# Kernel optimization log

Hardware: AMD Instinct MI355X
Metric: run time of the kernel (lower is better)

Reference implementation:

```python
import jax, jax.numpy as jnp
import numpy as np

NUM_CLASSES = 80
IOU_THR = 0.5
SCORE_THR = 0.3
K = 256              # per-class candidate pool (pre-NMS top-k)
MAX_PER_CLASS = 100  # max_output_size_per_class
MAX_TOTAL = 100      # max_total_size
NEG = -1e9


def _make_boxes(key, shape):
    kc, ks = jax.random.split(key)
    cyx = jax.random.uniform(kc, shape + (2,), dtype=jnp.float32)
    hw = jax.random.uniform(ks, shape + (2,), dtype=jnp.float32) * 0.2
    return jnp.concatenate([cyx - hw * 0.5, cyx + hw * 0.5], axis=-1)  # [y1,x1,y2,x2]


def setup_inputs() -> dict:
    key = jax.random.key(0)
    ks = jax.random.split(key, 9)
    B = 8
    inp = {}
    for i, g in enumerate([52, 26, 13]):
        inp[f"b{i+1}"] = _make_boxes(ks[3 * i], (B, g, g, 3))                       # (B,g,g,3,4)
        inp[f"c{i+1}"] = jax.random.uniform(ks[3 * i + 1], (B, g, g, 3, 1))          # objectness
        inp[f"p{i+1}"] = jax.random.uniform(ks[3 * i + 2], (B, g, g, 3, NUM_CLASSES))
    return inp


def _pairwise_iou(b):  # b: (K,4) in [y1,x1,y2,x2]
    y1, x1, y2, x2 = b[:, 0], b[:, 1], b[:, 2], b[:, 3]
    area = (y2 - y1) * (x2 - x1)
    iy = jnp.clip(jnp.minimum(y2[:, None], y2[None, :]) - jnp.maximum(y1[:, None], y1[None, :]), 0.0)
    ix = jnp.clip(jnp.minimum(x2[:, None], x2[None, :]) - jnp.maximum(x1[:, None], x1[None, :]), 0.0)
    inter = iy * ix
    union = area[:, None] + area[None, :] - inter
    return jnp.where(union > 0, inter / union, 0.0)


def _nms_one_class(boxes, scores):  # boxes (N,4), scores (N,)
    sc, idx = jax.lax.top_k(scores, K)
    b = boxes[idx]                      # (K,4) sorted by score desc
    valid = sc > SCORE_THR
    iou = _pairwise_iou(b)              # (K,K)
    rng = jnp.arange(K)

    def body(keep, i):
        cur = keep[i] & valid[i]
        keep = keep & ~(cur & (iou[i] > IOU_THR) & (rng > i))
        return keep, cur

    _, kept = jax.lax.scan(body, jnp.ones(K, dtype=bool), rng)
    kept = kept & (jnp.cumsum(kept) <= MAX_PER_CLASS)
    return b, jnp.where(kept, sc, NEG)  # (K,4), (K,)


def _combined_nms(boxes, scores):  # boxes (B,N,4), scores (B,N,C)
    per_class = jax.vmap(_nms_one_class, in_axes=(None, 1))   # over classes
    per_image = jax.vmap(per_class, in_axes=(0, 0))           # over batch
    cb, cs = per_image(boxes, scores)                         # (B,C,K,4), (B,C,K)
    B, C = scores.shape[0], scores.shape[2]
    flat_s = cs.reshape(B, C * K)
    flat_b = cb.reshape(B, C * K, 4)
    cls_ids = jnp.broadcast_to(jnp.arange(C, dtype=jnp.float32)[:, None], (C, K)).reshape(C * K)
    top_s, top_i = jax.lax.top_k(flat_s, MAX_TOTAL)           # global top-100
    top_b = jnp.take_along_axis(flat_b, top_i[:, :, None], axis=1)
    top_c = cls_ids[top_i]
    valid = top_s > SCORE_THR
    boxes_out = jnp.clip(jnp.where(valid[..., None], top_b, 0.0), 0.0, 1.0)  # clip_boxes=True
    scores_out = jnp.where(valid, top_s, 0.0)
    classes_out = jnp.where(valid, top_c, 0.0)
    nvalid = valid.sum(axis=-1).astype(jnp.int32)
    return boxes_out, scores_out, classes_out, nvalid


def reference(b1, c1, p1, b2, c2, p2, b3, c3, p3):
    B = b1.shape[0]
    bboxes = jnp.concatenate([b.reshape(B, -1, 4) for b in (b1, b2, b3)], axis=1)          # (B,N,4)
    conf = jnp.concatenate([c.reshape(B, -1, 1) for c in (c1, c2, c3)], axis=1)            # (B,N,1)
    cls = jnp.concatenate([p.reshape(B, -1, NUM_CLASSES) for p in (p1, p2, p3)], axis=1)   # (B,N,C)
    scores = conf * cls                                                                     # (B,N,C)
    return _combined_nms(bboxes, scores)
```

## Files before the change

### kernel.cpp

```cpp
#include <hip/hip_runtime.h>
#include <stdint.h>

#define BATCH 8
#define NC 80
#define NA1 8112
#define NA2 2028
#define NA3 507
#define NTOT 10647
#define TILE 64
#define NTILES 167
#define NSLOTS (NTILES*TILE)
#define KSEL 256
#define MAXPC 100
#define MAXTOT 100
#define SCTHR 0.3f
#define IOUTHR 0.5f
#define KEYTHR 0xBE99999Au
#define KEYBASE 0xBE99999Bu
#define STAGE_CAP 5120

typedef unsigned long long ull;

__device__ ull g_cand[(size_t)BATCH * NC * NSLOTS];
__device__ unsigned g_tcnt[BATCH * NC * NTILES];
__device__ ull g_ks[BATCH * NC * MAXPC];
__device__ unsigned g_kcnt[BATCH * NC];
__device__ ull g_ms[BATCH * 10 * MAXTOT];
__device__ unsigned g_mcnt[BATCH * 10];

__device__ __forceinline__ unsigned okey(float f) {
  unsigned u = __float_as_uint(f);
  return u ^ ((unsigned)((int)u >> 31) | 0x80000000u);
}
__device__ __forceinline__ float inv_okey(unsigned k) {
  unsigned u = (k & 0x80000000u) ? (k ^ 0x80000000u) : ~k;
  return __uint_as_float(u);
}
__device__ __forceinline__ ull shflxor64(ull v, int m) {
  int lo = __shfl_xor((int)(unsigned)v, m, 64);
  int hi = __shfl_xor((int)(unsigned)(v >> 32), m, 64);
  return ((ull)(unsigned)hi << 32) | (unsigned)lo;
}
__device__ __forceinline__ ull bcast64(ull v, int src) {
  int lo = __shfl((int)(unsigned)v, src, 64);
  int hi = __shfl((int)(unsigned)(v >> 32), src, 64);
  return ((ull)(unsigned)hi << 32) | (unsigned)lo;
}
__device__ __forceinline__ unsigned wave_sufscan(unsigned v, int lane) {
  #pragma unroll
  for (int off = 1; off < 64; off <<= 1) {
    unsigned t = __shfl_down(v, off, 64);
    if (lane + off < 64) v += t;
  }
  return v;
}

template <typename F>
__device__ void radix_sel24(F getkey, int n, unsigned kwant,
                            unsigned* hist4, unsigned* suf,
                            unsigned* s_sel, unsigned* wtot,
                            unsigned& T_out, unsigned& need_out)
{
  const int tid = threadIdx.x;
  const int lane = tid & 63, wv = tid >> 6;
  const int wb = wv << 8;
  unsigned need = kwant, prefix = 0;
  for (int shift = 16; shift >= 0; shift -= 8) {
    hist4[tid] = 0; hist4[tid + 256] = 0; hist4[tid + 512] = 0; hist4[tid + 768] = 0;
    __syncthreads();
    unsigned maskhi = (shift == 16) ? 0u : (0x00FFFFFFu ^ ((1u << (shift + 8)) - 1u));
    for (int i = tid; i < n; i += 256) {
      unsigned k = getkey(i);
      if (k != 0xFFFFFFFFu && (k & maskhi) == prefix)
        atomicAdd(&hist4[wb + ((k >> shift) & 255u)], 1u);
    }
    __syncthreads();
    unsigned v = hist4[tid] + hist4[tid + 256] + hist4[tid + 512] + hist4[tid + 768];
    v = wave_sufscan(v, lane);
    if (lane == 0) wtot[wv] = v;
    __syncthreads();
    unsigned add = 0;
    for (int w = wv + 1; w < 4; ++w) add += wtot[w];
    v += add;
    suf[tid] = v;
    __syncthreads();
    unsigned nxt = (tid == 255) ? 0u : suf[tid + 1];
    if (v >= need && nxt < need) {
      s_sel[0] = prefix | ((unsigned)tid << shift);
      s_sel[1] = need - nxt;
    }
    __syncthreads();
    prefix = s_sel[0]; need = s_sel[1];
    __syncthreads();
  }
  T_out = prefix; need_out = need;
}

__global__ __launch_bounds__(256)
void score_compact(const float* __restrict__ c1, const float* __restrict__ p1,
                   const float* __restrict__ c2, const float* __restrict__ p2,
                   const float* __restrict__ c3, const float* __restrict__ p3)
{
  const int tid = threadIdx.x;
  const int b = blockIdx.x / NTILES;
  const int t = blockIdx.x % NTILES;
  const int n0 = t * TILE;

  __shared__ float sp[TILE * 81];

  for (int e4 = tid; e4 < TILE * 20; e4 += 256) {
    int a = e4 / 20;
    int c4 = (e4 - a * 20) * 4;
    int ng = n0 + a;
    if (ng < NTOT) {
      const float* pp; int nl;
      if (ng < NA1)            { pp = p1 + (size_t)b * NA1 * NC; nl = ng; }
      else if (ng < NA1 + NA2) { pp = p2 + (size_t)b * NA2 * NC; nl = ng - NA1; }
      else                     { pp = p3 + (size_t)b * NA3 * NC; nl = ng - NA1 - NA2; }
      float4 pv = *(const float4*)(pp + (size_t)nl * NC + c4);
      sp[a * 81 + c4 + 0] = pv.x; sp[a * 81 + c4 + 1] = pv.y;
      sp[a * 81 + c4 + 2] = pv.z; sp[a * 81 + c4 + 3] = pv.w;
    }
  }
  __syncthreads();

  const int wv = tid >> 6, lane = tid & 63;
  const int ng = n0 + lane;
  const bool av = ng < NTOT;
  float cf = 0.0f;
  if (av) {
    if (ng < NA1)            cf = c1[b * NA1 + ng];
    else if (ng < NA1 + NA2) cf = c2[b * NA2 + ng - NA1];
    else                     cf = c3[b * NA3 + ng - NA1 - NA2];
  }
  for (int k = 0; k < 20; ++k) {
    int c = wv + 4 * k;
    float pv = av ? sp[lane * 81 + c] : 0.0f;
    unsigned key = okey(pv * cf);
    bool pred = av && (key > KEYTHR);
    ull m = __ballot(pred);
    if (pred) {
      unsigned pos = (unsigned)__popcll(m & ((1ull << lane) - 1ull));
      g_cand[((size_t)(b * NC + c) * NTILES + t) * TILE + pos] =
          ((ull)key << 32) | (unsigned)(~ng);
    }
    if (lane == 0) g_tcnt[(b * NC + c) * NTILES + t] = (unsigned)__popcll(m);
  }
}

__global__ __launch_bounds__(256)
void nms_per_class(const float* __restrict__ b1, const float* __restrict__ b2,
                   const float* __restrict__ b3)
{
  const int tid = threadIdx.x;
  const int lane = tid & 63, wv = tid >> 6;
  const int bc = blockIdx.x;
  const int b = bc / NC;
  const int c = bc - b * NC;

  __shared__ unsigned ckey[STAGE_CAP];
  __shared__ unsigned short cslot[STAGE_CAP];
  __shared__ ull uSupp[KSEL * 5];
  __shared__ float4 cbox[KSEL];
  __shared__ ull cand[KSEL];
  __shared__ ull kw[4], kfw[4];
  __shared__ unsigned s_sel[2], wtot[4];
  __shared__ int s_cgt, s_ceq;

  ull* supp = uSupp;
  unsigned* hist4 = (unsigned*)uSupp;
  unsigned* suf = (unsigned*)uSupp + 1024;
  unsigned* tc = (unsigned*)cbox;
  unsigned* off = (unsigned*)cbox + 168;

  const ull* crow = g_cand + (size_t)bc * NSLOTS;
  const unsigned* trow = g_tcnt + bc * NTILES;

  cand[tid] = 0ull;
  if (tid < NTILES) tc[tid] = trow[tid];
  __syncthreads();

  if (wv == 0) {
    unsigned carry = 0;
    for (int ch = 0; ch < 3; ++ch) {
      int idx = ch * 64 + lane;
      unsigned x = (idx < NTILES) ? tc[idx] : 0u;
      unsigned v = x;
      #pragma unroll
      for (int o = 1; o < 64; o <<= 1) {
        unsigned t2 = __shfl_up(v, o, 64);
        if (lane >= o) v += t2;
      }
      if (idx < NTILES) off[idx] = carry + v - x;
      carry += (unsigned)__shfl((int)v, 63, 64);
    }
    if (lane == 0) off[NTILES] = carry;
  }
  __syncthreads();
  const int cnt = (int)off[NTILES];
  const bool staged = (cnt > KSEL) && (cnt <= STAGE_CAP);

  for (int s = tid; s < NSLOTS; s += 256) {
    int t = s >> 6, j = s & 63;
    if (j < (int)tc[t]) {
      if (cnt <= KSEL) {
        cand[off[t] + j] = crow[s];
      } else if (staged) {
        int pos = off[t] + j;
        ckey[pos] = (unsigned)(crow[s] >> 32);
        cslot[pos] = (unsigned short)s;
      }
    }
  }
  __syncthreads();

  if (cnt > KSEL) {
    unsigned T, need;
    if (staged) {
      auto gk = [&](int i) { return ckey[i] - KEYBASE; };
      radix_sel24(gk, cnt, KSEL, hist4, suf, s_sel, wtot, T, need);
    } else {
      auto gk = [&](int s) {
        int t = s >> 6, j = s & 63;
        return (j < (int)tc[t]) ? ((unsigned)(crow[s] >> 32) - KEYBASE) : 0xFFFFFFFFu;
      };
      radix_sel24(gk, NSLOTS, KSEL, hist4, suf, s_sel, wtot, T, need);
    }
    if (tid == 0) { s_cgt = 0; s_ceq = 0; }
    __syncthreads();
    const int ngt = KSEL - (int)need;
    if (staged) {
      for (int i = tid; i < cnt; i += 256) {
        unsigned k = ckey[i] - KEYBASE;
        if (k > T) cand[atomicAdd(&s_cgt, 1)] = crow[cslot[i]];
        else if (k == T) { int p = atomicAdd(&s_ceq, 1); if (p < (int)need) cand[ngt + p] = crow[cslot[i]]; }
      }
    } else {
      for (int s = tid; s < NSLOTS; s += 256) {
        int t = s >> 6, j = s & 63;
        if (j < (int)tc[t]) {
          ull v = crow[s];
          unsigned k = (unsigned)(v >> 32) - KEYBASE;
          if (k > T) cand[atomicAdd(&s_cgt, 1)] = v;
          else if (k == T) { int p = atomicAdd(&s_ceq, 1); if (p < (int)need) cand[ngt + p] = v; }
        }
      }
    }
  }
  __syncthreads();

  ull v = cand[tid];
  for (int kk = 2; kk <= KSEL; kk <<= 1) {
    for (int j = kk >> 1; j > 0; j >>= 1) {
      ull o;
      if (j >= 64) {
        cand[tid] = v;
        __syncthreads();
        o = cand[tid ^ j];
        __syncthreads();
      } else {
        o = shflxor64(v, j);
      }
      bool keep_max = (((tid & j) == 0) == ((tid & kk) == 0));
      v = keep_max ? (v > o ? v : o) : (v < o ? v : o);
    }
  }
  __syncthreads();

  int myn = 0;
  {
    float4 bx = make_float4(0.f, 0.f, 0.f, 0.f);
    if (v != 0ull) {
      myn = (int)(~(unsigned)v);
      const float* bp;
      if (myn < NA1)            bp = b1 + (size_t)(b * NA1 + myn) * 4;
      else if (myn < NA1 + NA2) bp = b2 + (size_t)(b * NA2 + (myn - NA1)) * 4;
      else                      bp = b3 + (size_t)(b * NA3 + (myn - NA1 - NA2)) * 4;
      bx = make_float4(bp[0], bp[1], bp[2], bp[3]);
    }
    cbox[tid] = bx;
  }
  ull mvalid = __ballot(v != 0ull);
  if (lane == 0) kw[wv] = mvalid;
  __syncthreads();

  {
    const float4 mb = cbox[tid];
    const float myarea = (mb.z - mb.x) * (mb.w - mb.y);
    ull m0 = 0, m1 = 0, m2 = 0, m3 = 0;
    for (int j = 0; j < KSEL; ++j) {
      float4 bj = cbox[j];
      float ja = (bj.z - bj.x) * (bj.w - bj.y);
      float iy = fmaxf(fminf(bj.z, mb.z) - fmaxf(bj.x, mb.x), 0.0f);
      float ix = fmaxf(fminf(bj.w, mb.w) - fmaxf(bj.y, mb.y), 0.0f);
      float inter = iy * ix;
      float uni = ja + myarea - inter;
      bool sup = (j > tid) && (uni > 0.0f) && (inter > IOUTHR * uni);
      ull bit = sup ? (1ull << (j & 63)) : 0ull;
      if ((j >> 6) == 0) m0 |= bit; else if ((j >> 6) == 1) m1 |= bit;
      else if ((j >> 6) == 2) m2 |= bit; else m3 |= bit;
    }
    supp[tid * 5 + 0] = m0; supp[tid * 5 + 1] = m1;
    supp[tid * 5 + 2] = m2; supp[tid * 5 + 3] = m3;
  }
  __syncthreads();

  if (wv == 0) {
    ull r0[4], r1[4], r2[4], r3[4];
    #pragma unroll
    for (int w = 0; w < 4; ++w) {
      r0[w] = supp[(lane) * 5 + w];
      r1[w] = supp[(64 + lane) * 5 + w];
      r2[w] = supp[(128 + lane) * 5 + w];
      r3[w] = supp[(192 + lane) * 5 + w];
    }
    ull k0 = kw[0], k1 = kw[1], k2 = kw[2], k3 = kw[3];
    ull f0 = 0, f1 = 0, f2 = 0, f3 = 0;
    int run = 0;
#define SCAN_CHUNK(R, KT, FT)                                              \
    for (int ib = 0; ib < 64; ++ib) {                                      \
      if ((KT >> ib) & 1ull) {                                             \
        k0 &= ~bcast64(R[0], ib); k1 &= ~bcast64(R[1], ib);                \
        k2 &= ~bcast64(R[2], ib); k3 &= ~bcast64(R[3], ib);                \
        if (++run <= MAXPC) FT |= (1ull << ib);                            \
      }                                                                    \
    }
    SCAN_CHUNK(r0, k0, f0)
    SCAN_CHUNK(r1, k1, f1)
    SCAN_CHUNK(r2, k2, f2)
    SCAN_CHUNK(r3, k3, f3)
#undef SCAN_CHUNK
    if (lane == 0) { kfw[0] = f0; kfw[1] = f1; kfw[2] = f2; kfw[3] = f3; }
  }
  __syncthreads();

  {
    ull w0 = kfw[0], w1 = kfw[1], w2 = kfw[2], w3 = kfw[3];
    int wq = tid >> 6, wb2 = tid & 63;
    ull myw = (wq == 0) ? w0 : (wq == 1) ? w1 : (wq == 2) ? w2 : w3;
    bool kept = (myw >> wb2) & 1ull;
    if (kept) {
      ull lt = (wb2 == 0) ? 0ull : (myw & ((1ull << wb2) - 1ull));
      int rank = __popcll(lt);
      if (wq > 0) rank += __popcll(w0);
      if (wq > 1) rank += __popcll(w1);
      if (wq > 2) rank += __popcll(w2);
      unsigned key = (unsigned)(v >> 32);
      unsigned n = (~(unsigned)v) & 0x3FFFu;
      ull e = ((ull)(key - KEYBASE) << 40) | ((ull)(unsigned)(127 - c) << 33) |
              ((ull)(unsigned)(255 - tid) << 25) | n;
      g_ks[(size_t)bc * MAXPC + rank] = e;
    }
    if (tid == 0)
      g_kcnt[bc] = (unsigned)(__popcll(w0) + __popcll(w1) + __popcll(w2) + __popcll(w3));
  }
}

__global__ __launch_bounds__(256)
void nms_merge8()
{
  const int tid = threadIdx.x;
  const int b = blockIdx.x / 10, g = blockIdx.x % 10;
  __shared__ ull le[8 * MAXPC];
  __shared__ ull cand[128];
  __shared__ unsigned kc[8], ko[9];
  __shared__ unsigned hist4[1024], suf[256], s_sel[2], wtot[4];
  __shared__ int s_cgt, s_ceq;

  if (tid < 8) kc[tid] = g_kcnt[b * NC + g * 8 + tid];
  if (tid < 128) cand[tid] = 0ull;
  __syncthreads();
  if (tid == 0) { unsigned a = 0; for (int i = 0; i < 8; ++i) { ko[i] = a; a += kc[i]; } ko[8] = a; }
  __syncthreads();
  const int total = (int)ko[8];

  for (int s = tid; s < 8 * MAXPC; s += 256) {
    int c8 = s / MAXPC, j = s - c8 * MAXPC;
    if (j < (int)kc[c8]) le[ko[c8] + j] = g_ks[(size_t)(b * NC + g * 8 + c8) * MAXPC + j];
  }
  __syncthreads();

  if (total <= MAXTOT) {
    if (tid < total) cand[tid] = le[tid];
  } else {
    unsigned T, need;
    auto gk = [&](int i) { return (unsigned)(le[i] >> 40); };
    radix_sel24(gk, total, MAXTOT, hist4, suf, s_sel, wtot, T, need);
    if (tid == 0) { s_cgt = 0; s_ceq = 0; }
    __syncthreads();
    const int ngt = MAXTOT - (int)need;
    for (int i = tid; i < total; i += 256) {
      unsigned k = (unsigned)(le[i] >> 40);
      if (k > T) cand[atomicAdd(&s_cgt, 1)] = le[i];
      else if (k == T) { int p = atomicAdd(&s_ceq, 1); if (p < (int)need) cand[ngt + p] = le[i]; }
    }
  }
  __syncthreads();

  for (int kk = 2; kk <= 128; kk <<= 1) {
    for (int j = kk >> 1; j > 0; j >>= 1) {
      if (tid < 128) {
        int ixj = tid ^ j;
        if (ixj > tid) {
          ull a = cand[tid], c2 = cand[ixj];
          if (((tid & kk) == 0) ? (a < c2) : (a > c2)) { cand[tid] = c2; cand[ixj] = a; }
        }
      }
      __syncthreads();
    }
  }
  if (tid < MAXTOT) g_ms[(size_t)(b * 10 + g) * MAXTOT + tid] = cand[tid];
  if (tid == 0) g_mcnt[b * 10 + g] = (unsigned)(total < MAXTOT ? total : MAXTOT);
}

__global__ __launch_bounds__(256)
void nms_final(const float* __restrict__ b1, const float* __restrict__ b2,
               const float* __restrict__ b3, float* __restrict__ out)
{
  const int tid = threadIdx.x;
  const int b = blockIdx.x;
  __shared__ ull me[10 * MAXTOT];
  __shared__ ull cand[128];
  __shared__ unsigned mc[10], mo[11];
  __shared__ unsigned hist4[1024], suf[256], s_sel[2], wtot[4];
  __shared__ int s_cgt, s_ceq;

  if (tid < 10) mc[tid] = g_mcnt[b * 10 + tid];
  if (tid < 128) cand[tid] = 0ull;
  __syncthreads();
  if (tid == 0) { unsigned a = 0; for (int i = 0; i < 10; ++i) { mo[i] = a; a += mc[i]; } mo[10] = a; }
  __syncthreads();
  const int total = (int)mo[10];

  for (int s = tid; s < 10 * MAXTOT; s += 256) {
    int c10 = s / MAXTOT, j = s - c10 * MAXTOT;
    if (j < (int)mc[c10]) me[mo[c10] + j] = g_ms[(size_t)(b * 10 + c10) * MAXTOT + j];
  }
  __syncthreads();

  if (total <= MAXTOT) {
    if (tid < total) cand[tid] = me[tid];
  } else {
    unsigned T, need;
    auto gk = [&](int i) { return (unsigned)(me[i] >> 40); };
    radix_sel24(gk, total, MAXTOT, hist4, suf, s_sel, wtot, T, need);
    if (tid == 0) { s_cgt = 0; s_ceq = 0; }
    __syncthreads();
    const int ngt = MAXTOT - (int)need;
    for (int i = tid; i < total; i += 256) {
      unsigned k = (unsigned)(me[i] >> 40);
      if (k > T) cand[atomicAdd(&s_cgt, 1)] = me[i];
      else if (k == T) { int p = atomicAdd(&s_ceq, 1); if (p < (int)need) cand[ngt + p] = me[i]; }
    }
  }
  __syncthreads();

  for (int kk = 2; kk <= 128; kk <<= 1) {
    for (int j = kk >> 1; j > 0; j >>= 1) {
      if (tid < 128) {
        int ixj = tid ^ j;
        if (ixj > tid) {
          ull a = cand[tid], c2 = cand[ixj];
          if (((tid & kk) == 0) ? (a < c2) : (a > c2)) { cand[tid] = c2; cand[ixj] = a; }
        }
      }
      __syncthreads();
    }
  }

  if (tid < MAXTOT) {
    ull e = cand[tid];
    float o0 = 0.f, o1 = 0.f, o2 = 0.f, o3 = 0.f, osc = 0.f, ocl = 0.f;
    if (e != 0ull) {
      unsigned key24 = (unsigned)(e >> 40);
      float sc = inv_okey(key24 + KEYBASE);
      int cls = 127 - (int)((e >> 33) & 127u);
      int n = (int)(e & 0x3FFFu);
      const float* bp;
      if (n < NA1)            bp = b1 + (size_t)(b * NA1 + n) * 4;
      else if (n < NA1 + NA2) bp = b2 + (size_t)(b * NA2 + (n - NA1)) * 4;
      else                    bp = b3 + (size_t)(b * NA3 + (n - NA1 - NA2)) * 4;
      o0 = fminf(fmaxf(bp[0], 0.0f), 1.0f);
      o1 = fminf(fmaxf(bp[1], 0.0f), 1.0f);
      o2 = fminf(fmaxf(bp[2], 0.0f), 1.0f);
      o3 = fminf(fmaxf(bp[3], 0.0f), 1.0f);
      osc = sc; ocl = (float)cls;
    }
    int oi = b * MAXTOT + tid;
    out[(size_t)oi * 4 + 0] = o0;
    out[(size_t)oi * 4 + 1] = o1;
    out[(size_t)oi * 4 + 2] = o2;
    out[(size_t)oi * 4 + 3] = o3;
    out[BATCH * MAXTOT * 4 + oi] = osc;
    out[BATCH * MAXTOT * 5 + oi] = ocl;
  }
  if (tid == 0) out[BATCH * MAXTOT * 6 + b] = (float)(total < MAXTOT ? total : MAXTOT);
}

extern "C" void kernel_launch(void* const* d_in, const int* in_sizes, int n_in,
                              void* d_out, int out_size, void* d_ws, size_t ws_size,
                              hipStream_t stream) {
  const float* b1 = (const float*)d_in[0];
  const float* c1 = (const float*)d_in[1];
  const float* p1 = (const float*)d_in[2];
  const float* b2 = (const float*)d_in[3];
  const float* c2 = (const float*)d_in[4];
  const float* p2 = (const float*)d_in[5];
  const float* b3 = (const float*)d_in[6];
  const float* c3 = (const float*)d_in[7];
  const float* p3 = (const float*)d_in[8];
  (void)in_sizes; (void)n_in; (void)out_size; (void)d_ws; (void)ws_size;

  score_compact<<<dim3(BATCH * NTILES), dim3(256), 0, stream>>>(c1, p1, c2, p2, c3, p3);
  nms_per_class<<<dim3(BATCH * NC), dim3(256), 0, stream>>>(b1, b2, b3);
  nms_merge8<<<dim3(BATCH * 10), dim3(256), 0, stream>>>();
  nms_final<<<dim3(BATCH), dim3(256), 0, stream>>>(b1, b2, b3, (float*)d_out);
}
```

Measured before the change: 241.7 us.

## Fuse merge stage into final kernel and restructure per-class candidate staging

Drops the intermediate merge kernel, so the final kernel now gathers all 80 per-class kept lists per image and runs one radix select over up to 8000 entries. In the per-class kernel, the key/slot staging arrays are replaced by a full 64-bit staging buffer, which removes the second global re-read of candidates. Global loads are batched eight at a time, and the scatter uses wave-aggregated atomics instead of per-thread atomics. The keep-scan now exits early once 100 boxes are kept, and a few loops get unroll pragmas. The trade-off is fewer launches and fewer global reads against an 8-block final stage with more serial work per block, plus less parallelism at the end.

```diff
diff --git a/kernel.cpp b/kernel.cpp
--- a/kernel.cpp
+++ b/kernel.cpp
@@ -17,7 +17,7 @@
 #define IOUTHR 0.5f
 #define KEYTHR 0xBE99999Au
 #define KEYBASE 0xBE99999Bu
-#define STAGE_CAP 5120
+#define STAGE_CAP 4608
 
 typedef unsigned long long ull;
 
@@ -25,8 +25,6 @@
 __device__ unsigned g_tcnt[BATCH * NC * NTILES];
 __device__ ull g_ks[BATCH * NC * MAXPC];
 __device__ unsigned g_kcnt[BATCH * NC];
-__device__ ull g_ms[BATCH * 10 * MAXTOT];
-__device__ unsigned g_mcnt[BATCH * 10];
 
 __device__ __forceinline__ unsigned okey(float f) {
   unsigned u = __float_as_uint(f);
@@ -69,6 +67,7 @@
     hist4[tid] = 0; hist4[tid + 256] = 0; hist4[tid + 512] = 0; hist4[tid + 768] = 0;
     __syncthreads();
     unsigned maskhi = (shift == 16) ? 0u : (0x00FFFFFFu ^ ((1u << (shift + 8)) - 1u));
+    #pragma unroll 4
     for (int i = tid; i < n; i += 256) {
       unsigned k = getkey(i);
       if (k != 0xFFFFFFFFu && (k & maskhi) == prefix)
@@ -158,25 +157,23 @@
   const int b = bc / NC;
   const int c = bc - b * NC;
 
-  __shared__ unsigned ckey[STAGE_CAP];
-  __shared__ unsigned short cslot[STAGE_CAP];
-  __shared__ ull uSupp[KSEL * 5];
-  __shared__ float4 cbox[KSEL];
+  __shared__ ull cstage[STAGE_CAP];
+  __shared__ unsigned tc[NTILES];
+  __shared__ unsigned off[NTILES + 1];
+  __shared__ unsigned hist4[1024];
+  __shared__ unsigned suf[256];
   __shared__ ull cand[KSEL];
   __shared__ ull kw[4], kfw[4];
   __shared__ unsigned s_sel[2], wtot[4];
   __shared__ int s_cgt, s_ceq;
-
-  ull* supp = uSupp;
-  unsigned* hist4 = (unsigned*)uSupp;
-  unsigned* suf = (unsigned*)uSupp + 1024;
-  unsigned* tc = (unsigned*)cbox;
-  unsigned* off = (unsigned*)cbox + 168;
+  ull* supp = cstage;
+  float4* cbox = (float4*)((char*)cstage + 10240);
 
   const ull* crow = g_cand + (size_t)bc * NSLOTS;
   const unsigned* trow = g_tcnt + bc * NTILES;
 
   cand[tid] = 0ull;
+  if (tid == 0) { s_cgt = 0; s_ceq = 0; }
   if (tid < NTILES) tc[tid] = trow[tid];
   __syncthreads();
 
@@ -200,15 +197,22 @@
   const int cnt = (int)off[NTILES];
   const bool staged = (cnt > KSEL) && (cnt <= STAGE_CAP);
 
-  for (int s = tid; s < NSLOTS; s += 256) {
-    int t = s >> 6, j = s & 63;
-    if (j < (int)tc[t]) {
-      if (cnt <= KSEL) {
-        cand[off[t] + j] = crow[s];
-      } else if (staged) {
-        int pos = off[t] + j;
-        ckey[pos] = (unsigned)(crow[s] >> 32);
-        cslot[pos] = (unsigned short)s;
+  for (int base = 0; base < NSLOTS; base += 2048) {
+    ull v[8]; int pos[8]; bool ok[8];
+    #pragma unroll
+    for (int e = 0; e < 8; ++e) {
+      int s = base + e * 256 + tid;
+      ok[e] = false;
+      if (s < NSLOTS) {
+        int t = s >> 6, j = s & 63;
+        if (j < (int)tc[t]) { ok[e] = true; pos[e] = (int)off[t] + j; v[e] = crow[s]; }
+      }
+    }
+    #pragma unroll
+    for (int e = 0; e < 8; ++e) {
+      if (ok[e]) {
+        if (cnt <= KSEL) cand[pos[e]] = v[e];
+        else if (staged) cstage[pos[e]] = v[e];
       }
     }
   }
@@ -217,7 +221,7 @@
   if (cnt > KSEL) {
     unsigned T, need;
     if (staged) {
-      auto gk = [&](int i) { return ckey[i] - KEYBASE; };
+      auto gk = [&](int i) { return (unsigned)(cstage[i] >> 32) - KEYBASE; };
       radix_sel24(gk, cnt, KSEL, hist4, suf, s_sel, wtot, T, need);
     } else {
       auto gk = [&](int s) {
@@ -226,14 +230,25 @@
       };
       radix_sel24(gk, NSLOTS, KSEL, hist4, suf, s_sel, wtot, T, need);
     }
-    if (tid == 0) { s_cgt = 0; s_ceq = 0; }
-    __syncthreads();
     const int ngt = KSEL - (int)need;
     if (staged) {
-      for (int i = tid; i < cnt; i += 256) {
-        unsigned k = ckey[i] - KEYBASE;
-        if (k > T) cand[atomicAdd(&s_cgt, 1)] = crow[cslot[i]];
-        else if (k == T) { int p = atomicAdd(&s_ceq, 1); if (p < (int)need) cand[ngt + p] = crow[cslot[i]]; }
+      const int cntPad = (cnt + 255) & ~255;
+      for (int i = tid; i < cntPad; i += 256) {
+        ull v = (i < cnt) ? cstage[i] : 0ull;
+        unsigned k = (unsigned)(v >> 32) - KEYBASE;
+        bool g = (i < cnt) && (k > T);
+        bool q = (i < cnt) && (k == T);
+        ull mg = __ballot(g), mq = __ballot(q);
+        unsigned bg = 0, bq = 0;
+        if (lane == 0) {
+          if (mg) bg = (unsigned)atomicAdd(&s_cgt, (int)__popcll(mg));
+          if (mq) bq = (unsigned)atomicAdd(&s_ceq, (int)__popcll(mq));
+        }
+        bg = (unsigned)__shfl((int)bg, 0, 64);
+        bq = (unsigned)__shfl((int)bq, 0, 64);
+        ull lt = (1ull << lane) - 1ull;
+        if (g) cand[bg + __popcll(mg & lt)] = v;
+        if (q) { int p = (int)(bq + __popcll(mq & lt)); if (p < (int)need) cand[ngt + p] = v; }
       }
     } else {
       for (int s = tid; s < NSLOTS; s += 256) {
@@ -267,11 +282,10 @@
   }
   __syncthreads();
 
-  int myn = 0;
   {
     float4 bx = make_float4(0.f, 0.f, 0.f, 0.f);
     if (v != 0ull) {
-      myn = (int)(~(unsigned)v);
+      int myn = (int)(~(unsigned)v);
       const float* bp;
       if (myn < NA1)            bp = b1 + (size_t)(b * NA1 + myn) * 4;
       else if (myn < NA1 + NA2) bp = b2 + (size_t)(b * NA2 + (myn - NA1)) * 4;
@@ -288,6 +302,7 @@
     const float4 mb = cbox[tid];
     const float myarea = (mb.z - mb.x) * (mb.w - mb.y);
     ull m0 = 0, m1 = 0, m2 = 0, m3 = 0;
+    #pragma unroll 8
     for (int j = 0; j < KSEL; ++j) {
       float4 bj = cbox[j];
       float ja = (bj.z - bj.x) * (bj.w - bj.y);
@@ -318,11 +333,12 @@
     ull f0 = 0, f1 = 0, f2 = 0, f3 = 0;
     int run = 0;
 #define SCAN_CHUNK(R, KT, FT)                                              \
-    for (int ib = 0; ib < 64; ++ib) {                                      \
+    if (KT) for (int ib = 0; ib < 64; ++ib) {                              \
       if ((KT >> ib) & 1ull) {                                             \
         k0 &= ~bcast64(R[0], ib); k1 &= ~bcast64(R[1], ib);                \
         k2 &= ~bcast64(R[2], ib); k3 &= ~bcast64(R[3], ib);                \
-        if (++run <= MAXPC) FT |= (1ull << ib);                            \
+        FT |= (1ull << ib);                                                \
+        if (++run == MAXPC) goto scan_done;                                \
       }                                                                    \
     }
     SCAN_CHUNK(r0, k0, f0)
@@ -330,6 +346,7 @@
     SCAN_CHUNK(r2, k2, f2)
     SCAN_CHUNK(r3, k3, f3)
 #undef SCAN_CHUNK
+scan_done:
     if (lane == 0) { kfw[0] = f0; kfw[1] = f1; kfw[2] = f2; kfw[3] = f3; }
   }
   __syncthreads();
@@ -357,26 +374,46 @@
 }
 
 __global__ __launch_bounds__(256)
-void nms_merge8()
+void nms_final(const float* __restrict__ b1, const float* __restrict__ b2,
+               const float* __restrict__ b3, float* __restrict__ out)
 {
   const int tid = threadIdx.x;
-  const int b = blockIdx.x / 10, g = blockIdx.x % 10;
-  __shared__ ull le[8 * MAXPC];
+  const int lane = tid & 63, wv = tid >> 6;
+  const int b = blockIdx.x;
+  __shared__ ull le[NC * MAXPC];
   __shared__ ull cand[128];
-  __shared__ unsigned kc[8], ko[9];
+  __shared__ unsigned kc[NC], ko[NC + 1];
   __shared__ unsigned hist4[1024], suf[256], s_sel[2], wtot[4];
   __shared__ int s_cgt, s_ceq;
 
-  if (tid < 8) kc[tid] = g_kcnt[b * NC + g * 8 + tid];
+  if (tid < NC) kc[tid] = g_kcnt[b * NC + tid];
   if (tid < 128) cand[tid] = 0ull;
-  __syncthreads();
-  if (tid == 0) { unsigned a = 0; for (int i = 0; i < 8; ++i) { ko[i] = a; a += kc[i]; } ko[8] = a; }
-  __syncthreads();
-  const int total = (int)ko[8];
-
-  for (int s = tid; s < 8 * MAXPC; s += 256) {
+  if (tid == 0) { s_cgt = 0; s_ceq = 0; }
+  __syncthreads();
+
+  if (wv == 0) {
+    unsigned carry = 0;
+    for (int ch = 0; ch < 2; ++ch) {
+      int idx = ch * 64 + lane;
+      unsigned x = (idx < NC) ? kc[idx] : 0u;
+      unsigned v = x;
+      #pragma unroll
+      for (int o = 1; o < 64; o <<= 1) {
+        unsigned t2 = __shfl_up(v, o, 64);
+        if (lane >= o) v += t2;
+      }
+      if (idx < NC) ko[idx] = carry + v - x;
+      carry += (unsigned)__shfl((int)v, 63, 64);
+    }
+    if (lane == 0) ko[NC] = carry;
+  }
+  __syncthreads();
+  const int total = (int)ko[NC];
+
+  #pragma unroll 4
+  for (int s = tid; s < NC * MAXPC; s += 256) {
     int c8 = s / MAXPC, j = s - c8 * MAXPC;
-    if (j < (int)kc[c8]) le[ko[c8] + j] = g_ks[(size_t)(b * NC + g * 8 + c8) * MAXPC + j];
+    if (j < (int)kc[c8]) le[ko[c8] + j] = g_ks[(size_t)(b * NC + c8) * MAXPC + j];
   }
   __syncthreads();
 
@@ -386,71 +423,24 @@
     unsigned T, need;
     auto gk = [&](int i) { return (unsigned)(le[i] >> 40); };
     radix_sel24(gk, total, MAXTOT, hist4, suf, s_sel, wtot, T, need);
-    if (tid == 0) { s_cgt = 0; s_ceq = 0; }
-    __syncthreads();
     const int ngt = MAXTOT - (int)need;
-    for (int i = tid; i < total; i += 256) {
-      unsigned k = (unsigned)(le[i] >> 40);
-      if (k > T) cand[atomicAdd(&s_cgt, 1)] = le[i];
-      else if (k == T) { int p = atomicAdd(&s_ceq, 1); if (p < (int)need) cand[ngt + p] = le[i]; }
-    }
-  }
-  __syncthreads();
-
-  for (int kk = 2; kk <= 128; kk <<= 1) {
-    for (int j = kk >> 1; j > 0; j >>= 1) {
-      if (tid < 128) {
-        int ixj = tid ^ j;
-        if (ixj > tid) {
-          ull a = cand[tid], c2 = cand[ixj];
-          if (((tid & kk) == 0) ? (a < c2) : (a > c2)) { cand[tid] = c2; cand[ixj] = a; }
-        }
-      }
-      __syncthreads();
-    }
-  }
-  if (tid < MAXTOT) g_ms[(size_t)(b * 10 + g) * MAXTOT + tid] = cand[tid];
-  if (tid == 0) g_mcnt[b * 10 + g] = (unsigned)(total < MAXTOT ? total : MAXTOT);
-}
-
-__global__ __launch_bounds__(256)
-void nms_final(const float* __restrict__ b1, const float* __restrict__ b2,
-               const float* __restrict__ b3, float* __restrict__ out)
-{
-  const int tid = threadIdx.x;
-  const int b = blockIdx.x;
-  __shared__ ull me[10 * MAXTOT];
-  __shared__ ull cand[128];
-  __shared__ unsigned mc[10], mo[11];
-  __shared__ unsigned hist4[1024], suf[256], s_sel[2], wtot[4];
-  __shared__ int s_cgt, s_ceq;
-
-  if (tid < 10) mc[tid] = g_mcnt[b * 10 + tid];
-  if (tid < 128) cand[tid] = 0ull;
-  __syncthreads();
-  if (tid == 0) { unsigned a = 0; for (int i = 0; i < 10; ++i) { mo[i] = a; a += mc[i]; } mo[10] = a; }
-  __syncthreads();
-  const int total = (int)mo[10];
-
-  for (int s = tid; s < 10 * MAXTOT; s += 256) {
-    int c10 = s / MAXTOT, j = s - c10 * MAXTOT;
-    if (j < (int)mc[c10]) me[mo[c10] + j] = g_ms[(size_t)(b * 10 + c10) * MAXTOT + j];
-  }
-  __syncthreads();
-
-  if (total <= MAXTOT) {
-    if (tid < total) cand[tid] = me[tid];
-  } else {
-    unsigned T, need;
-    auto gk = [&](int i) { return (unsigned)(me[i] >> 40); };
-    radix_sel24(gk, total, MAXTOT, hist4, suf, s_sel, wtot, T, need);
-    if (tid == 0) { s_cgt = 0; s_ceq = 0; }
-    __syncthreads();
-    const int ngt = MAXTOT - (int)need;
-    for (int i = tid; i < total; i += 256) {
-      unsigned k = (unsigned)(me[i] >> 40);
-      if (k > T) cand[atomicAdd(&s_cgt, 1)] = me[i];
-      else if (k == T) { int p = atomicAdd(&s_ceq, 1); if (p < (int)need) cand[ngt + p] = me[i]; }
+    const int totPad = (total + 255) & ~255;
+    for (int i = tid; i < totPad; i += 256) {
+      ull v = (i < total) ? le[i] : 0ull;
+      unsigned k = (unsigned)(v >> 40);
+      bool g = (i < total) && (k > T);
+      bool q = (i < total) && (k == T);
+      ull mg = __ballot(g), mq = __ballot(q);
+      unsigned bg = 0, bq = 0;
+      if (lane == 0) {
+        if (mg) bg = (unsigned)atomicAdd(&s_cgt, (int)__popcll(mg));
+        if (mq) bq = (unsigned)atomicAdd(&s_ceq, (int)__popcll(mq));
+      }
+      bg = (unsigned)__shfl((int)bg, 0, 64);
+      bq = (unsigned)__shfl((int)bq, 0, 64);
+      ull lt = (1ull << lane) - 1ull;
+      if (g) cand[bg + __popcll(mg & lt)] = v;
+      if (q) { int p = (int)(bq + __popcll(mq & lt)); if (p < (int)need) cand[ngt + p] = v; }
     }
   }
   __syncthreads();
@@ -513,6 +503,5 @@
 
   score_compact<<<dim3(BATCH * NTILES), dim3(256), 0, stream>>>(c1, p1, c2, p2, c3, p3);
   nms_per_class<<<dim3(BATCH * NC), dim3(256), 0, stream>>>(b1, b2, b3);
-  nms_merge8<<<dim3(BATCH * 10), dim3(256), 0, stream>>>();
   nms_final<<<dim3(BATCH), dim3(256), 0, stream>>>(b1, b2, b3, (float*)d_out);
 }
```

New measurement: 227.8 us. 5.8% less time.
